# Kernel tuning notes

Measured on AMD Instinct MI355X. Metric: run time of the kernel, lower is better.

Reference implementation:

```python
import jax, jax.numpy as jnp
import numpy as np

NE = 14          # NUM_ELEMENTS
NC = 20          # NUM_CHANNEL
DEN = NE         # density channel
GRV = NE + 1     # gravity channel

# (id, density, gravity) per element, in id order
_ELEMS = [(0,1,1),(1,4,0),(2,3,1),(3,2,1),(4,0,1),(5,4,0),(6,4,0),(7,0,1),(8,4,0),(9,3,1),(10,3,1),(11,2,1),(12,3,1),(13,4,0)]

def _elem_table():
    t = np.zeros((NE, NC), dtype=np.float32)
    for eid, dens, grav in _ELEMS:
        t[eid, eid] = 1.0
        t[eid, DEN] = dens
        t[eid, GRV] = grav
    return jnp.asarray(t)

# torch.roll semantics: get_above(x)[h] = x[h-1] (wrap)
above = lambda x: jnp.roll(x, 1, axis=2)
below = lambda x: jnp.roll(x, -1, axis=2)
left  = lambda x: jnp.roll(x, 1, axis=3)
right = lambda x: jnp.roll(x, -1, axis=3)

def interp2(sa, sb, if_false, if_a, if_b):
    # faithful to torch: (~a & ~b)*f + a*xa + b*xb (bools broadcast-multiply floats)
    return (jnp.logical_and(~sa, ~sb)) * if_false + sa * if_a + sb * if_b

def setup_inputs() -> dict:
    key = jax.random.key(0)
    k1, k2 = jax.random.split(key)
    B, H, W = 8, 512, 512
    ids = jax.random.randint(k1, (B, H, W), 0, NE)
    world = _elem_table()[ids]                 # [B,H,W,NC]
    world = jnp.transpose(world, (0, 3, 1, 2)) # [B,NC,H,W]
    rand_movement = jax.random.uniform(k2, (B, 1, H, W), dtype=jnp.float32)
    return {"world": world, "rand_movement": rand_movement}

def reference(world, rand_movement):
    B, C, H, W = world.shape
    # --- stone support check (conv2d with zero padding, taps at top-left/top-right) ---
    stone = world[:, 9:10]
    p = jnp.pad(stone, ((0, 0), (0, 0), (1, 1), (1, 1)))
    supports = p[:, :, 0:H, 0:W] + p[:, :, 0:H, 2:W + 2]  # stone[h-1,w-1]+stone[h-1,w+1]
    new_grav = (1.0 - stone) * world[:, GRV:GRV + 1] + stone * (supports < 2)
    world = world.at[:, GRV:GRV + 1].set(new_grav)

    # --- vertical gravity passes over densities 0..3 ---
    did_gravity = jnp.zeros((B, 1, H, W), dtype=world.dtype)
    for curr_density in (0, 1, 2, 3):
        density = world[:, DEN:DEN + 1]
        is_density_above_greater = (above(density) - density) > 0
        is_density_below_less = below(is_density_above_greater)
        is_density_current = density == curr_density
        is_density_above_current = above(is_density_current)
        is_gravity = world[:, GRV:GRV + 1] == 1
        is_cb_gravity = jnp.logical_and(below(is_gravity), is_gravity)
        is_ca_gravity = jnp.logical_and(above(is_gravity), is_gravity)
        does_become_below = is_density_current & is_density_below_less & is_cb_gravity
        does_become_above = is_density_above_greater & is_density_above_current & is_ca_gravity
        did_gravity = did_gravity + does_become_above
        world = interp2(does_become_below, does_become_above, world, below(world), above(world))

    # --- diagonal fall for sand (2) and dust (12) ---
    for elem in (2, 12):
        fall_dir = rand_movement > 0.5
        not_did_gravity = did_gravity <= 0
        for fall_left in (True, False):
            g_dir = left if fall_left else right
            g_not = right if fall_left else left
            is_element = world[:, elem:elem + 1] == 1
            is_ar_element = g_not(above(is_element))
            density = world[:, DEN:DEN + 1]
            is_matching_fall = fall_dir if fall_left else ~fall_dir
            is_ar_matching_fall = g_not(above(is_matching_fall))
            is_bl_density_lower = (density - g_dir(below(density))) > 0
            is_ar_density_higher = (g_not(above(density)) - density) > 0
            is_gravity = world[:, GRV:GRV + 1] == 1
            is_bl_gravity = jnp.logical_and(g_dir(below(is_gravity)), is_gravity)
            is_ar_gravity = jnp.logical_and(g_not(above(is_gravity)), is_gravity)
            ndg_bl = jnp.logical_and(g_dir(below(not_did_gravity)), not_did_gravity)
            ndg_ar = jnp.logical_and(g_not(above(not_did_gravity)), not_did_gravity)
            does_become_bl = is_element & ndg_bl & is_matching_fall & is_bl_density_lower & is_bl_gravity
            does_become_ar = is_ar_element & ndg_ar & is_ar_matching_fall & is_ar_density_higher & is_ar_gravity
            world = interp2(does_become_bl, does_become_ar, world, g_dir(below(world)), g_not(above(world)))
    return world
```

## Files before the change

kernel.cpp:

```cpp
#include <hip/hip_runtime.h>
#include <stdint.h>

#define HH 512
#define WW 512
#define PLANE (HH*WW)
#define NCH 20

#define GRAV_PACK 0x1E9Du

__device__ __forceinline__ void bar_lds() {
    __builtin_amdgcn_sched_barrier(0);
    asm volatile("s_waitcnt lgkmcnt(0)" ::: "memory");
    __builtin_amdgcn_s_barrier();
    __builtin_amdgcn_sched_barrier(0);
}

__device__ __forceinline__ uint32_t eqz4(uint32_t x) {
    uint32_t nz = (x | (x >> 1) | (x >> 2) | (x >> 3)) & 0x01010101u;
    return nz ^ 0x01010101u;
}
__device__ __forceinline__ uint32_t bmask(uint32_t b) {
    uint32_t h = b << 7;
    return (h - (h >> 7)) | h;
}

__device__ __forceinline__ uint32_t pack_cell(float d_,
                                              float c1_, float c5_, float c6_, float c8_,
                                              float c2_, float c9_, float c10_,
                                              float c3_, float c4_) {
    int d = (int)d_;
    int e;
    if (d == 4)      e = (c1_ != 0.f) ? 1 : (c5_ != 0.f) ? 5 : (c6_ != 0.f) ? 6 : (c8_ != 0.f) ? 8 : 13;
    else if (d == 3) e = (c2_ != 0.f) ? 2 : (c9_ != 0.f) ? 9 : (c10_ != 0.f) ? 10 : 12;
    else if (d == 2) e = (c3_ != 0.f) ? 3 : 11;
    else if (d == 1) e = 0;
    else             e = (c4_ != 0.f) ? 4 : 7;
    int g = (int)((GRAV_PACK >> e) & 1u);
    return (uint32_t)(e | (g << 4) | (d << 5));
}

__global__ __launch_bounds__(256) void extract_k(const float* __restrict__ world,
                                                 uint32_t* __restrict__ st) {
    int idx = blockIdx.x * 256 + threadIdx.x;
    int b  = idx >> 16;
    int p4 = idx & 0xFFFF;
    const float4* base = (const float4*)(world + (size_t)b * NCH * PLANE) + p4;
    float4 vD  = base[14 * (PLANE / 4)];
    float4 v1  = base[ 1 * (PLANE / 4)];
    float4 v5  = base[ 5 * (PLANE / 4)];
    float4 v6  = base[ 6 * (PLANE / 4)];
    float4 v8  = base[ 8 * (PLANE / 4)];
    float4 v2  = base[ 2 * (PLANE / 4)];
    float4 v9  = base[ 9 * (PLANE / 4)];
    float4 v10 = base[10 * (PLANE / 4)];
    float4 v3  = base[ 3 * (PLANE / 4)];
    float4 v4  = base[ 4 * (PLANE / 4)];
    uint32_t b0 = pack_cell(vD.x, v1.x, v5.x, v6.x, v8.x, v2.x, v9.x, v10.x, v3.x, v4.x);
    uint32_t b1 = pack_cell(vD.y, v1.y, v5.y, v6.y, v8.y, v2.y, v9.y, v10.y, v3.y, v4.y);
    uint32_t b2 = pack_cell(vD.z, v1.z, v5.z, v6.z, v8.z, v2.z, v9.z, v10.z, v3.z, v4.z);
    uint32_t b3 = pack_cell(vD.w, v1.w, v5.w, v6.w, v8.w, v2.w, v9.w, v10.w, v3.w, v4.w);
    st[idx] = b0 | (b1 << 8) | (b2 << 16) | (b3 << 24);
}

#define TILE_R 32
#define TILE_C 64
#define HALO_T 9
#define HALO_B 8
#define HALO_W 8
#define RH (TILE_R + HALO_T + HALO_B)
#define RWW 20
#define RWS 21
#define NW (RH*RWW)
#define NT 512
#define NOWN 2

__global__ __launch_bounds__(NT, 4) void sim_k(const uint8_t* __restrict__ st_in,
                                               const float* __restrict__ rnd,
                                               float* __restrict__ out) {
    __shared__ uint32_t bufA[RH * RWS];
    __shared__ uint32_t bufB[RH * RWS];
    __shared__ uint32_t aux [RH * RWS];

    const int tid = threadIdx.x;
    const int h0  = blockIdx.y * TILE_R;
    const int w0  = blockIdx.x * TILE_C;

    uint32_t sreg[NOWN], freg[NOWN], dgreg[NOWN];

    auto stage = [&](const uint8_t* stb, const float* rb) {
#pragma unroll
        for (int k = 0; k < NOWN; ++k) {
            int r = tid + k * NT;
            if (r < NW) {
                int i = r / RWW, jw = r - i * RWW;
                int gh  = (h0 + i - HALO_T) & (HH - 1);
                int gwb = (w0 + jw * 4 - HALO_W) & (WW - 1);
                uint32_t w = *(const uint32_t*)(stb + gh * WW + gwb);
                bufA[i * RWS + jw] = w;
                sreg[k] = w;
                float4 rv = *(const float4*)(rb + gh * WW + gwb);
                uint32_t aw = 0;
                aw |= (rv.x > 0.5f) ? 0x00000001u : 0u;
                aw |= (rv.y > 0.5f) ? 0x00000100u : 0u;
                aw |= (rv.z > 0.5f) ? 0x00010000u : 0u;
                aw |= (rv.w > 0.5f) ? 0x01000000u : 0u;
                freg[k] = aw;
                dgreg[k] = 0u;
            }
        }
    };

    auto passes = [&]() {
#pragma unroll
        for (int k = 0; k < NOWN; ++k) {
            int r = tid + k * NT;
            if (r < NW) {
                int i = r / RWW, jw = r - i * RWW;
                uint32_t s = sreg[k];
                uint32_t stm = eqz4((s & 0x0F0F0F0Fu) ^ 0x09090909u);
                int im = (i > 0) ? i - 1 : 0;
                int jl = (jw > 0) ? jw - 1 : 0;
                int jr = (jw < RWW - 1) ? jw + 1 : RWW - 1;
                uint32_t wU  = bufA[im * RWS + jw];
                uint32_t wUL = bufA[im * RWS + jl];
                uint32_t wUR = bufA[im * RWS + jr];
                uint32_t upL = (wU << 8) | (wUL >> 24);
                uint32_t upR = (wU >> 8) | (wUR << 24);
                uint32_t stL = eqz4((upL & 0x0F0F0F0Fu) ^ 0x09090909u);
                uint32_t stR = eqz4((upR & 0x0F0F0F0Fu) ^ 0x09090909u);
                int gh  = (h0 + i - HALO_T) & (HH - 1);
                int gwb = (w0 + jw * 4 - HALO_W) & (WW - 1);
                uint32_t rowOK = (gh != 0) ? 0x01010101u : 0u;
                uint32_t okL = 0x01010101u ^ ((gwb == 0)      ? 0x00000001u : 0u);
                uint32_t okR = 0x01010101u ^ ((gwb == WW - 4) ? 0x01000000u : 0u);
                uint32_t supL = stL & okL & rowOK;
                uint32_t supR = stR & okR & rowOK;
                uint32_t g2 = 0x01010101u ^ (supL & supR);
                uint32_t ns = (s & ~0x10101010u) | (g2 << 4);
                uint32_t res = s ^ ((s ^ ns) & bmask(stm));
                bufB[i * RWS + jw] = res;
                sreg[k] = res;
            }
        }
        bar_lds();

        uint32_t* cur = bufB;
        uint32_t* nxt = bufA;

#pragma unroll
        for (int curr = 0; curr < 4; ++curr) {
            const uint32_t crep = (uint32_t)curr * 0x01010101u;
            const uint32_t CKP7 = crep + 0x0F0F0F0Fu;
#pragma unroll
            for (int k = 0; k < NOWN; ++k) {
                int r = tid + k * NT;
                if (r < NW) {
                    int i = r / RWW, jw = r - i * RWW;
                    int ia = (i > 0) ? i - 1 : 0;
                    int ib = (i < RH - 1) ? i + 1 : RH - 1;
                    uint32_t s  = sreg[k];
                    uint32_t sa = cur[ia * RWS + jw];
                    uint32_t sb = cur[ib * RWS + jw];
                    uint32_t d  = (s  >> 5) & 0x07070707u;
                    uint32_t da = (sa >> 5) & 0x07070707u;
                    uint32_t db = (sb >> 5) & 0x07070707u;
                    uint32_t g  = (s  >> 4) & 0x01010101u;
                    uint32_t ga = (sa >> 4) & 0x01010101u;
                    uint32_t gb = (sb >> 4) & 0x01010101u;
                    uint32_t bel = eqz4(d ^ crep)  & (((CKP7 - db) & 0x10101010u) >> 4) & gb & g;
                    uint32_t abv = eqz4(da ^ crep) & (((CKP7 - d)  & 0x10101010u) >> 4) & ga & g;
                    uint32_t res = s ^ ((s ^ sb) & bmask(bel)) ^ ((s ^ sa) & bmask(abv));
                    nxt[i * RWS + jw] = res;
                    sreg[k] = res;
                    dgreg[k] |= abv;
                    if (curr == 3)
                        aux[i * RWS + jw] = freg[k] | (dgreg[k] << 1);
                }
            }
            bar_lds();
            uint32_t* t = cur; cur = nxt; nxt = t;
        }

#pragma unroll
        for (int pass = 0; pass < 4; ++pass) {
            const int  elem = (pass < 2) ? 2 : 12;
            const bool fl   = ((pass & 1) == 0);
            const uint32_t erep = (uint32_t)elem * 0x01010101u;
#pragma unroll
            for (int k = 0; k < NOWN; ++k) {
                int r = tid + k * NT;
                if (r < NW) {
                    int i = r / RWW, jw = r - i * RWW;
                    int ia = (i > 0) ? i - 1 : 0;
                    int ib = (i < RH - 1) ? i + 1 : RH - 1;
                    int jl = (jw > 0) ? jw - 1 : 0;
                    int jr = (jw < RWW - 1) ? jw + 1 : RWW - 1;
                    uint32_t s  = sreg[k];
                    uint32_t wB = cur[ib * RWS + jw];
                    uint32_t wA = cur[ia * RWS + jw];
                    uint32_t aB = aux[ib * RWS + jw];
                    uint32_t aA = aux[ia * RWS + jw];
                    uint32_t sbl, sar, abl, aar;
                    if (fl) {
                        uint32_t wBL = cur[ib * RWS + jl], wAR = cur[ia * RWS + jr];
                        uint32_t aBL = aux[ib * RWS + jl], aAR = aux[ia * RWS + jr];
                        sbl = (wB << 8) | (wBL >> 24);
                        sar = (wA >> 8) | (wAR << 24);
                        abl = (aB << 8) | (aBL >> 24);
                        aar = (aA >> 8) | (aAR << 24);
                    } else {
                        uint32_t wBR = cur[ib * RWS + jr], wAL = cur[ia * RWS + jl];
                        uint32_t aBR = aux[ib * RWS + jr], aAL = aux[ia * RWS + jl];
                        sbl = (wB >> 8) | (wBR << 24);
                        sar = (wA << 8) | (wAL >> 24);
                        abl = (aB >> 8) | (aBR << 24);
                        aar = (aA << 8) | (aAL >> 24);
                    }
                    uint32_t d   = (s   >> 5) & 0x07070707u;
                    uint32_t dbl = (sbl >> 5) & 0x07070707u;
                    uint32_t dar = (sar >> 5) & 0x07070707u;
                    uint32_t g   = (s   >> 4) & 0x01010101u;
                    uint32_t gbl = (sbl >> 4) & 0x01010101u;
                    uint32_t gar = (sar >> 4) & 0x01010101u;
                    uint32_t ndg   = dgreg[k] ^ 0x01010101u;
                    uint32_t ndgbl = ((~abl) >> 1) & 0x01010101u;
                    uint32_t ndgar = ((~aar) >> 1) & 0x01010101u;
                    uint32_t mtc = (fl ? freg[k] : ~freg[k]) & 0x01010101u;
                    uint32_t mta = (fl ? aar : ~aar) & 0x01010101u;
                    uint32_t eqe  = eqz4((s   & 0x0F0F0F0Fu) ^ erep);
                    uint32_t eqer = eqz4((sar & 0x0F0F0F0Fu) ^ erep);
                    uint32_t bbl = eqe  & ndgbl & ndg & mtc & (((0x12121212u - dbl) & 0x10101010u) >> 4) & gbl & g;
                    uint32_t bar = eqer & ndgar & ndg & mta & (((0x12121212u - d)   & 0x10101010u) >> 4) & gar & g;
                    uint32_t res = s ^ ((s ^ sbl) & bmask(bbl)) ^ ((s ^ sar) & bmask(bar));
                    nxt[i * RWS + jw] = res;
                    sreg[k] = res;
                }
            }
            bar_lds();
            uint32_t* t = cur; cur = nxt; nxt = t;
        }
    };

    auto expand = [&](float* ob, uint32_t w) {
        float* base = ob + (size_t)(h0 + (tid >> 4)) * WW + (w0 + (tid & 15) * 4);
        uint32_t oh0 = 1u << ( w        & 15u);
        uint32_t oh1 = 1u << ((w >>  8) & 15u);
        uint32_t oh2 = 1u << ((w >> 16) & 15u);
        uint32_t oh3 = 1u << ((w >> 24) & 15u);
#pragma unroll
        for (int c = 0; c < 14; ++c) {
            float4 v;
            v.x = (float)((oh0 >> c) & 1u);
            v.y = (float)((oh1 >> c) & 1u);
            v.z = (float)((oh2 >> c) & 1u);
            v.w = (float)((oh3 >> c) & 1u);
            *(float4*)(base + (size_t)c * PLANE) = v;
        }
        float4 vd = { (float)((w >>  5) & 7u), (float)((w >> 13) & 7u),
                      (float)((w >> 21) & 7u), (float)((w >> 29) & 7u) };
        *(float4*)(base + (size_t)14 * PLANE) = vd;
        float4 vg = { (float)((w >>  4) & 1u), (float)((w >> 12) & 1u),
                      (float)((w >> 20) & 1u), (float)((w >> 28) & 1u) };
        *(float4*)(base + (size_t)15 * PLANE) = vg;
        float4 z = {0.f, 0.f, 0.f, 0.f};
#pragma unroll
        for (int c = 16; c < 20; ++c)
            *(float4*)(base + (size_t)c * PLANE) = z;
    };

    const int bA = blockIdx.z, bB = blockIdx.z + 4;
    const uint8_t* stA = st_in + (size_t)bA * PLANE;
    const uint8_t* stB = st_in + (size_t)bB * PLANE;
    const float*   rA  = rnd   + (size_t)bA * PLANE;
    const float*   rB  = rnd   + (size_t)bB * PLANE;
    float* obA = out + (size_t)bA * NCH * PLANE;
    float* obB = out + (size_t)bB * NCH * PLANE;

    const int coreIdx = (HALO_T + (tid >> 4)) * RWS + (HALO_W / 4) + (tid & 15);

    stage(stA, rA);
    bar_lds();
    passes();

    uint32_t wA = bufB[coreIdx];
    stage(stB, rB);
    expand(obA, wA);
    bar_lds();
    passes();

    expand(obB, bufB[coreIdx]);
}

extern "C" void kernel_launch(void* const* d_in, const int* in_sizes, int n_in,
                              void* d_out, int out_size, void* d_ws, size_t ws_size,
                              hipStream_t stream) {
    const float* world = (const float*)d_in[0];
    const float* rnd   = (const float*)d_in[1];
    float* out = (float*)d_out;
    uint32_t* st = (uint32_t*)d_ws;

    extract_k<<<2048, 256, 0, stream>>>(world, st);

    dim3 grid(WW / TILE_C, HH / TILE_R, 4);
    sim_k<<<grid, NT, 0, stream>>>((const uint8_t*)st, rnd, out);
}
```

Baseline: 55.49 us.

## Give each wavefront its own tile to replace block barriers with wave-local fences

```diff
diff --git a/kernel.cpp b/kernel.cpp
--- a/kernel.cpp
+++ b/kernel.cpp
@@ -5,13 +5,11 @@
 #define WW 512
 #define PLANE (HH*WW)
 #define NCH 20
-
 #define GRAV_PACK 0x1E9Du
 
-__device__ __forceinline__ void bar_lds() {
+__device__ __forceinline__ void wfence() {
     __builtin_amdgcn_sched_barrier(0);
     asm volatile("s_waitcnt lgkmcnt(0)" ::: "memory");
-    __builtin_amdgcn_s_barrier();
     __builtin_amdgcn_sched_barrier(0);
 }
 
@@ -62,187 +60,199 @@
     st[idx] = b0 | (b1 << 8) | (b2 << 16) | (b3 << 24);
 }
 
-#define TILE_R 32
-#define TILE_C 64
+#define TILE_R 16
 #define HALO_T 9
 #define HALO_B 8
 #define HALO_W 8
 #define RH (TILE_R + HALO_T + HALO_B)
 #define RWW 20
-#define RWS 21
 #define NW (RH*RWW)
-#define NT 512
-#define NOWN 2
-
-__global__ __launch_bounds__(NT, 4) void sim_k(const uint8_t* __restrict__ st_in,
-                                               const float* __restrict__ rnd,
-                                               float* __restrict__ out) {
-    __shared__ uint32_t bufA[RH * RWS];
-    __shared__ uint32_t bufB[RH * RWS];
-    __shared__ uint32_t aux [RH * RWS];
-
-    const int tid = threadIdx.x;
-    const int h0  = blockIdx.y * TILE_R;
-    const int w0  = blockIdx.x * TILE_C;
-
-    uint32_t sreg[NOWN], freg[NOWN], dgreg[NOWN];
-
-    auto stage = [&](const uint8_t* stb, const float* rb) {
-#pragma unroll
-        for (int k = 0; k < NOWN; ++k) {
-            int r = tid + k * NT;
-            if (r < NW) {
-                int i = r / RWW, jw = r - i * RWW;
-                int gh  = (h0 + i - HALO_T) & (HH - 1);
-                int gwb = (w0 + jw * 4 - HALO_W) & (WW - 1);
-                uint32_t w = *(const uint32_t*)(stb + gh * WW + gwb);
-                bufA[i * RWS + jw] = w;
-                sreg[k] = w;
+#define NOWN 11
+
+__global__ __launch_bounds__(256, 2) void sim_k(const uint8_t* __restrict__ st_in,
+                                                const float* __restrict__ rnd,
+                                                float* __restrict__ out) {
+    __shared__ uint32_t bufA[4 * NW];
+    __shared__ uint32_t bufB[4 * NW];
+    __shared__ uint32_t auxS[4 * NW];
+
+    const int tid  = threadIdx.x;
+    const int lane = tid & 63;
+    const int wid  = tid >> 6;
+    const int b    = blockIdx.z;
+    const int h0   = (blockIdx.y * 4 + wid) * TILE_R;
+    const int w0   = blockIdx.x * 64;
+
+    const uint8_t* stb = st_in + (size_t)b * PLANE;
+    const float*   rb  = rnd   + (size_t)b * PLANE;
+    float*         ob  = out   + (size_t)b * NCH * PLANE;
+
+    uint32_t* bA = bufA + wid * NW;
+    uint32_t* bB = bufB + wid * NW;
+    uint32_t* ax = auxS + wid * NW;
+
+#pragma unroll 1
+    for (int k = 0; k < NOWN; ++k) {
+        int r = lane + k * 64;
+        if (r < NW) {
+            int i = r / RWW, jw = r - i * RWW;
+            int gh  = (h0 + i - HALO_T) & (HH - 1);
+            int gwb = (w0 + jw * 4 - HALO_W) & (WW - 1);
+            bA[r] = *(const uint32_t*)(stb + gh * WW + gwb);
+            uint32_t aw = 0;
+            if (i >= HALO_T - 4 && i < RH - HALO_B + 4) {
                 float4 rv = *(const float4*)(rb + gh * WW + gwb);
-                uint32_t aw = 0;
                 aw |= (rv.x > 0.5f) ? 0x00000001u : 0u;
                 aw |= (rv.y > 0.5f) ? 0x00000100u : 0u;
                 aw |= (rv.z > 0.5f) ? 0x00010000u : 0u;
                 aw |= (rv.w > 0.5f) ? 0x01000000u : 0u;
-                freg[k] = aw;
-                dgreg[k] = 0u;
             }
-        }
-    };
-
-    auto passes = [&]() {
-#pragma unroll
+            ax[r] = aw;
+        }
+    }
+
+    {
+        float4 z = {0.f, 0.f, 0.f, 0.f};
+#pragma unroll
+        for (int q = 0; q < 4; ++q) {
+            int ci = lane + q * 64;
+            float* base = ob + (size_t)(h0 + (ci >> 4)) * WW + (w0 + (ci & 15) * 4);
+#pragma unroll
+            for (int c = 16; c < 20; ++c)
+                *(float4*)(base + (size_t)c * PLANE) = z;
+        }
+    }
+    wfence();
+
+#pragma unroll 1
+    for (int k = 0; k < NOWN; ++k) {
+        int r = lane + k * 64;
+        if (r < NW) {
+            int i = r / RWW, jw = r - i * RWW;
+            uint32_t s = bA[r];
+            uint32_t stm = eqz4((s & 0x0F0F0F0Fu) ^ 0x09090909u);
+            int rU  = (i > 0) ? r - RWW : r;
+            int rUL = (jw > 0) ? rU - 1 : rU;
+            int rUR = (jw < RWW - 1) ? rU + 1 : rU;
+            uint32_t wU  = bA[rU];
+            uint32_t wUL = bA[rUL];
+            uint32_t wUR = bA[rUR];
+            uint32_t upL = (wU << 8) | (wUL >> 24);
+            uint32_t upR = (wU >> 8) | (wUR << 24);
+            uint32_t stL = eqz4((upL & 0x0F0F0F0Fu) ^ 0x09090909u);
+            uint32_t stR = eqz4((upR & 0x0F0F0F0Fu) ^ 0x09090909u);
+            int gh  = (h0 + i - HALO_T) & (HH - 1);
+            int gwb = (w0 + jw * 4 - HALO_W) & (WW - 1);
+            uint32_t rowOK = (gh != 0) ? 0x01010101u : 0u;
+            uint32_t okL = 0x01010101u ^ ((gwb == 0)      ? 0x00000001u : 0u);
+            uint32_t okR = 0x01010101u ^ ((gwb == WW - 4) ? 0x01000000u : 0u);
+            uint32_t supL = stL & okL & rowOK;
+            uint32_t supR = stR & okR & rowOK;
+            uint32_t g2 = 0x01010101u ^ (supL & supR);
+            uint32_t ns = (s & ~0x10101010u) | (g2 << 4);
+            bB[r] = s ^ ((s ^ ns) & bmask(stm));
+        }
+    }
+    wfence();
+
+    uint32_t* cur = bB;
+    uint32_t* nxt = bA;
+
+#pragma unroll 1
+    for (int curr = 0; curr < 4; ++curr) {
+        const uint32_t crep = (uint32_t)curr * 0x01010101u;
+        const uint32_t CKP7 = crep + 0x0F0F0F0Fu;
+#pragma unroll 1
         for (int k = 0; k < NOWN; ++k) {
-            int r = tid + k * NT;
+            int r = lane + k * 64;
+            if (r < NW) {
+                int i = r / RWW;
+                int ra = (i > 0) ? r - RWW : r;
+                int rb2 = (i < RH - 1) ? r + RWW : r;
+                uint32_t s  = cur[r];
+                uint32_t sa = cur[ra];
+                uint32_t sb = cur[rb2];
+                uint32_t d  = (s  >> 5) & 0x07070707u;
+                uint32_t da = (sa >> 5) & 0x07070707u;
+                uint32_t db = (sb >> 5) & 0x07070707u;
+                uint32_t g  = (s  >> 4) & 0x01010101u;
+                uint32_t ga = (sa >> 4) & 0x01010101u;
+                uint32_t gb = (sb >> 4) & 0x01010101u;
+                uint32_t bel = eqz4(d ^ crep)  & (((CKP7 - db) & 0x10101010u) >> 4) & gb & g;
+                uint32_t abv = eqz4(da ^ crep) & (((CKP7 - d)  & 0x10101010u) >> 4) & ga & g;
+                nxt[r] = s ^ ((s ^ sb) & bmask(bel)) ^ ((s ^ sa) & bmask(abv));
+                if (abv) ax[r] |= (abv << 1);
+            }
+        }
+        wfence();
+        uint32_t* t = cur; cur = nxt; nxt = t;
+    }
+
+#pragma unroll 1
+    for (int pass = 0; pass < 4; ++pass) {
+        const int  elem = (pass < 2) ? 2 : 12;
+        const bool fl   = ((pass & 1) == 0);
+        const uint32_t erep = (uint32_t)elem * 0x01010101u;
+#pragma unroll 1
+        for (int k = 0; k < NOWN; ++k) {
+            int r = lane + k * 64;
             if (r < NW) {
                 int i = r / RWW, jw = r - i * RWW;
-                uint32_t s = sreg[k];
-                uint32_t stm = eqz4((s & 0x0F0F0F0Fu) ^ 0x09090909u);
-                int im = (i > 0) ? i - 1 : 0;
-                int jl = (jw > 0) ? jw - 1 : 0;
-                int jr = (jw < RWW - 1) ? jw + 1 : RWW - 1;
-                uint32_t wU  = bufA[im * RWS + jw];
-                uint32_t wUL = bufA[im * RWS + jl];
-                uint32_t wUR = bufA[im * RWS + jr];
-                uint32_t upL = (wU << 8) | (wUL >> 24);
-                uint32_t upR = (wU >> 8) | (wUR << 24);
-                uint32_t stL = eqz4((upL & 0x0F0F0F0Fu) ^ 0x09090909u);
-                uint32_t stR = eqz4((upR & 0x0F0F0F0Fu) ^ 0x09090909u);
-                int gh  = (h0 + i - HALO_T) & (HH - 1);
-                int gwb = (w0 + jw * 4 - HALO_W) & (WW - 1);
-                uint32_t rowOK = (gh != 0) ? 0x01010101u : 0u;
-                uint32_t okL = 0x01010101u ^ ((gwb == 0)      ? 0x00000001u : 0u);
-                uint32_t okR = 0x01010101u ^ ((gwb == WW - 4) ? 0x01000000u : 0u);
-                uint32_t supL = stL & okL & rowOK;
-                uint32_t supR = stR & okR & rowOK;
-                uint32_t g2 = 0x01010101u ^ (supL & supR);
-                uint32_t ns = (s & ~0x10101010u) | (g2 << 4);
-                uint32_t res = s ^ ((s ^ ns) & bmask(stm));
-                bufB[i * RWS + jw] = res;
-                sreg[k] = res;
+                int rA2 = (i > 0) ? r - RWW : r;
+                int rB2 = (i < RH - 1) ? r + RWW : r;
+                uint32_t s  = cur[r];
+                uint32_t wB = cur[rB2];
+                uint32_t wA = cur[rA2];
+                uint32_t aB = ax[rB2];
+                uint32_t aA = ax[rA2];
+                uint32_t axo = ax[r];
+                uint32_t sbl, sar, abl, aar;
+                if (fl) {
+                    int rBL = (jw > 0) ? rB2 - 1 : rB2;
+                    int rAR = (jw < RWW - 1) ? rA2 + 1 : rA2;
+                    uint32_t wBL = cur[rBL], wAR = cur[rAR];
+                    uint32_t aBL = ax[rBL],  aAR = ax[rAR];
+                    sbl = (wB << 8) | (wBL >> 24);
+                    sar = (wA >> 8) | (wAR << 24);
+                    abl = (aB << 8) | (aBL >> 24);
+                    aar = (aA >> 8) | (aAR << 24);
+                } else {
+                    int rBR = (jw < RWW - 1) ? rB2 + 1 : rB2;
+                    int rAL = (jw > 0) ? rA2 - 1 : rA2;
+                    uint32_t wBR = cur[rBR], wAL = cur[rAL];
+                    uint32_t aBR = ax[rBR],  aAL = ax[rAL];
+                    sbl = (wB >> 8) | (wBR << 24);
+                    sar = (wA << 8) | (wAL >> 24);
+                    abl = (aB >> 8) | (aBR << 24);
+                    aar = (aA << 8) | (aAL >> 24);
+                }
+                uint32_t d   = (s   >> 5) & 0x07070707u;
+                uint32_t dbl = (sbl >> 5) & 0x07070707u;
+                uint32_t g   = (s   >> 4) & 0x01010101u;
+                uint32_t gbl = (sbl >> 4) & 0x01010101u;
+                uint32_t gar = (sar >> 4) & 0x01010101u;
+                uint32_t ndg   = ((~axo) >> 1) & 0x01010101u;
+                uint32_t ndgbl = ((~abl) >> 1) & 0x01010101u;
+                uint32_t ndgar = ((~aar) >> 1) & 0x01010101u;
+                uint32_t mtc = (fl ? axo : ~axo) & 0x01010101u;
+                uint32_t mta = (fl ? aar : ~aar) & 0x01010101u;
+                uint32_t eqe  = eqz4((s   & 0x0F0F0F0Fu) ^ erep);
+                uint32_t eqer = eqz4((sar & 0x0F0F0F0Fu) ^ erep);
+                uint32_t bbl = eqe  & ndgbl & ndg & mtc & (((0x12121212u - dbl) & 0x10101010u) >> 4) & gbl & g;
+                uint32_t bar = eqer & ndgar & ndg & mta & (((0x12121212u - d)   & 0x10101010u) >> 4) & gar & g;
+                nxt[r] = s ^ ((s ^ sbl) & bmask(bbl)) ^ ((s ^ sar) & bmask(bar));
             }
         }
-        bar_lds();
-
-        uint32_t* cur = bufB;
-        uint32_t* nxt = bufA;
-
-#pragma unroll
-        for (int curr = 0; curr < 4; ++curr) {
-            const uint32_t crep = (uint32_t)curr * 0x01010101u;
-            const uint32_t CKP7 = crep + 0x0F0F0F0Fu;
-#pragma unroll
-            for (int k = 0; k < NOWN; ++k) {
-                int r = tid + k * NT;
-                if (r < NW) {
-                    int i = r / RWW, jw = r - i * RWW;
-                    int ia = (i > 0) ? i - 1 : 0;
-                    int ib = (i < RH - 1) ? i + 1 : RH - 1;
-                    uint32_t s  = sreg[k];
-                    uint32_t sa = cur[ia * RWS + jw];
-                    uint32_t sb = cur[ib * RWS + jw];
-                    uint32_t d  = (s  >> 5) & 0x07070707u;
-                    uint32_t da = (sa >> 5) & 0x07070707u;
-                    uint32_t db = (sb >> 5) & 0x07070707u;
-                    uint32_t g  = (s  >> 4) & 0x01010101u;
-                    uint32_t ga = (sa >> 4) & 0x01010101u;
-                    uint32_t gb = (sb >> 4) & 0x01010101u;
-                    uint32_t bel = eqz4(d ^ crep)  & (((CKP7 - db) & 0x10101010u) >> 4) & gb & g;
-                    uint32_t abv = eqz4(da ^ crep) & (((CKP7 - d)  & 0x10101010u) >> 4) & ga & g;
-                    uint32_t res = s ^ ((s ^ sb) & bmask(bel)) ^ ((s ^ sa) & bmask(abv));
-                    nxt[i * RWS + jw] = res;
-                    sreg[k] = res;
-                    dgreg[k] |= abv;
-                    if (curr == 3)
-                        aux[i * RWS + jw] = freg[k] | (dgreg[k] << 1);
-                }
-            }
-            bar_lds();
-            uint32_t* t = cur; cur = nxt; nxt = t;
-        }
-
-#pragma unroll
-        for (int pass = 0; pass < 4; ++pass) {
-            const int  elem = (pass < 2) ? 2 : 12;
-            const bool fl   = ((pass & 1) == 0);
-            const uint32_t erep = (uint32_t)elem * 0x01010101u;
-#pragma unroll
-            for (int k = 0; k < NOWN; ++k) {
-                int r = tid + k * NT;
-                if (r < NW) {
-                    int i = r / RWW, jw = r - i * RWW;
-                    int ia = (i > 0) ? i - 1 : 0;
-                    int ib = (i < RH - 1) ? i + 1 : RH - 1;
-                    int jl = (jw > 0) ? jw - 1 : 0;
-                    int jr = (jw < RWW - 1) ? jw + 1 : RWW - 1;
-                    uint32_t s  = sreg[k];
-                    uint32_t wB = cur[ib * RWS + jw];
-                    uint32_t wA = cur[ia * RWS + jw];
-                    uint32_t aB = aux[ib * RWS + jw];
-                    uint32_t aA = aux[ia * RWS + jw];
-                    uint32_t sbl, sar, abl, aar;
-                    if (fl) {
-                        uint32_t wBL = cur[ib * RWS + jl], wAR = cur[ia * RWS + jr];
-                        uint32_t aBL = aux[ib * RWS + jl], aAR = aux[ia * RWS + jr];
-                        sbl = (wB << 8) | (wBL >> 24);
-                        sar = (wA >> 8) | (wAR << 24);
-                        abl = (aB << 8) | (aBL >> 24);
-                        aar = (aA >> 8) | (aAR << 24);
-                    } else {
-                        uint32_t wBR = cur[ib * RWS + jr], wAL = cur[ia * RWS + jl];
-                        uint32_t aBR = aux[ib * RWS + jr], aAL = aux[ia * RWS + jl];
-                        sbl = (wB >> 8) | (wBR << 24);
-                        sar = (wA << 8) | (wAL >> 24);
-                        abl = (aB >> 8) | (aBR << 24);
-                        aar = (aA << 8) | (aAL >> 24);
-                    }
-                    uint32_t d   = (s   >> 5) & 0x07070707u;
-                    uint32_t dbl = (sbl >> 5) & 0x07070707u;
-                    uint32_t dar = (sar >> 5) & 0x07070707u;
-                    uint32_t g   = (s   >> 4) & 0x01010101u;
-                    uint32_t gbl = (sbl >> 4) & 0x01010101u;
-                    uint32_t gar = (sar >> 4) & 0x01010101u;
-                    uint32_t ndg   = dgreg[k] ^ 0x01010101u;
-                    uint32_t ndgbl = ((~abl) >> 1) & 0x01010101u;
-                    uint32_t ndgar = ((~aar) >> 1) & 0x01010101u;
-                    uint32_t mtc = (fl ? freg[k] : ~freg[k]) & 0x01010101u;
-                    uint32_t mta = (fl ? aar : ~aar) & 0x01010101u;
-                    uint32_t eqe  = eqz4((s   & 0x0F0F0F0Fu) ^ erep);
-                    uint32_t eqer = eqz4((sar & 0x0F0F0F0Fu) ^ erep);
-                    uint32_t bbl = eqe  & ndgbl & ndg & mtc & (((0x12121212u - dbl) & 0x10101010u) >> 4) & gbl & g;
-                    uint32_t bar = eqer & ndgar & ndg & mta & (((0x12121212u - d)   & 0x10101010u) >> 4) & gar & g;
-                    uint32_t res = s ^ ((s ^ sbl) & bmask(bbl)) ^ ((s ^ sar) & bmask(bar));
-                    nxt[i * RWS + jw] = res;
-                    sreg[k] = res;
-                }
-            }
-            bar_lds();
-            uint32_t* t = cur; cur = nxt; nxt = t;
-        }
-    };
-
-    auto expand = [&](float* ob, uint32_t w) {
-        float* base = ob + (size_t)(h0 + (tid >> 4)) * WW + (w0 + (tid & 15) * 4);
+        wfence();
+        uint32_t* t = cur; cur = nxt; nxt = t;
+    }
+
+#pragma unroll
+    for (int q = 0; q < 4; ++q) {
+        int ci = lane + q * 64;
+        int r  = (HALO_T + (ci >> 4)) * RWW + (HALO_W / 4) + (ci & 15);
+        uint32_t w = cur[r];
+        float* base = ob + (size_t)(h0 + (ci >> 4)) * WW + (w0 + (ci & 15) * 4);
         uint32_t oh0 = 1u << ( w        & 15u);
         uint32_t oh1 = 1u << ((w >>  8) & 15u);
         uint32_t oh2 = 1u << ((w >> 16) & 15u);
@@ -262,33 +272,7 @@
         float4 vg = { (float)((w >>  4) & 1u), (float)((w >> 12) & 1u),
                       (float)((w >> 20) & 1u), (float)((w >> 28) & 1u) };
         *(float4*)(base + (size_t)15 * PLANE) = vg;
-        float4 z = {0.f, 0.f, 0.f, 0.f};
-#pragma unroll
-        for (int c = 16; c < 20; ++c)
-            *(float4*)(base + (size_t)c * PLANE) = z;
-    };
-
-    const int bA = blockIdx.z, bB = blockIdx.z + 4;
-    const uint8_t* stA = st_in + (size_t)bA * PLANE;
-    const uint8_t* stB = st_in + (size_t)bB * PLANE;
-    const float*   rA  = rnd   + (size_t)bA * PLANE;
-    const float*   rB  = rnd   + (size_t)bB * PLANE;
-    float* obA = out + (size_t)bA * NCH * PLANE;
-    float* obB = out + (size_t)bB * NCH * PLANE;
-
-    const int coreIdx = (HALO_T + (tid >> 4)) * RWS + (HALO_W / 4) + (tid & 15);
-
-    stage(stA, rA);
-    bar_lds();
-    passes();
-
-    uint32_t wA = bufB[coreIdx];
-    stage(stB, rB);
-    expand(obA, wA);
-    bar_lds();
-    passes();
-
-    expand(obB, bufB[coreIdx]);
+    }
 }
 
 extern "C" void kernel_launch(void* const* d_in, const int* in_sizes, int n_in,
@@ -301,6 +285,6 @@
 
     extract_k<<<2048, 256, 0, stream>>>(world, st);
 
-    dim3 grid(WW / TILE_C, HH / TILE_R, 4);
-    sim_k<<<grid, NT, 0, stream>>>((const uint8_t*)st, rnd, out);
-}
+    dim3 grid(WW / 64, (HH / TILE_R) / 4, 8);
+    sim_k<<<grid, 256, 0, stream>>>((const uint8_t*)st, rnd, out);
+}
```

Result: slower. 70.98 us (+27.9%).
